# Performance work log

Measured on AMD Instinct MI355X. Metric: run time of the kernel, lower is better.

The kernel has to match this reference:

```python
import jax, jax.numpy as jnp
import numpy as np

# opt constants baked from init_kwargs
OPT_M = 1024      # number of OFDM subcarriers (opt.M)
N_PILOT = 0       # opt.N_pilot
VELOCITY = 100.0  # opt.V (is_random_v=False)
DECAY = 4.0       # opt.decay
C_LIGHT = 3.0e8
CARRIER_FREQ = 3.0e9


def setup_inputs() -> dict:
    key = jax.random.key(0)
    k1, k2 = jax.random.split(key, 2)
    N, P, L, M, S = 16, 4, 16, OPT_M, 128
    # channel tap power profile: exp(-l/decay), normalized
    power = jnp.exp(-jnp.arange(L, dtype=jnp.float32) / DECAY)
    power = power / jnp.sum(power)
    # Rayleigh(sigma=1) samples = sqrt(g1^2 + g2^2), g_i ~ N(0,1)
    g = jax.random.normal(k1, (N, P, L, 2), dtype=jnp.float32)
    rayleigh = jnp.sqrt(g[..., 0] ** 2 + g[..., 1] ** 2)
    cof = jnp.sqrt(power / 2.0) * rayleigh  # (N,P,L), strictly positive
    input_ri = jax.random.normal(k2, (N, P, S * M, 2), dtype=jnp.float32)
    return {"input_ri": input_ri, "cof": cof, "Ns": 128}


def reference(input_ri, cof, Ns):
    N, P, SMK, _ = input_ri.shape
    L = cof.shape[-1]
    S = Ns + N_PILOT  # OFDM mode: S = Ns + N_pilot, M = opt.M
    Mk = SMK // S
    x = (input_ri[..., 0] + 1j * input_ri[..., 1]).astype(jnp.complex64)  # (N,P,SMK)

    # per-tap propagation delay from tap gain: len = -100*log(cof); delay1 = len/c
    delay1 = (-100.0 * jnp.log(cof)) / C_LIGHT                      # (N,P,L)
    delay2 = jnp.linspace(0.0, (S - 1) * (0.0005 / 14.0), S).astype(jnp.float32)  # (S,)
    delay = delay1[..., None] + delay2                              # (N,P,L,S)

    max_doppler = VELOCITY / C_LIGHT * CARRIER_FREQ
    angles = jnp.linspace(0.0, 2.0 * np.pi, L).astype(jnp.float32)  # (L,)
    phase_coef = (2.0 * np.pi * jnp.cos(angles) * max_doppler)      # (L,)
    phases = phase_coef[None, None, :, None] * delay                # (N,P,L,S)
    shift = jnp.exp(-1j * phases.astype(jnp.float32))               # complex64 (N,P,L,S)

    # sum over taps L BEFORE multiplying by the L-independent input (same math,
    # avoids materializing the (N,P,L,S,M) broadcast intermediate)
    factor = jnp.sum(cof[..., None].astype(jnp.complex64) * shift, axis=2)  # (N,P,S)
    out = x.reshape(N, P, S, Mk) * factor[..., None]                # (N,P,S,M)
    out = out.reshape(N, P, SMK)
    out_ri = jnp.stack([out.real, out.imag], axis=-1)               # (N,P,SMK,2)

    # frequency response H_t = FFT of zero-padded taps
    cof_zp = jnp.concatenate([cof, jnp.zeros((N, P, OPT_M - L), cof.dtype)], axis=-1)
    H_t = jnp.fft.fft(cof_zp.astype(jnp.complex64), axis=-1)        # (N,P,OPT_M)
    H_t_ri = jnp.stack([H_t.real, H_t.imag], axis=-1)
    return out_ri, H_t_ri
```

## Files before the change

kernel.cpp:

```cpp
#include <hip/hip_runtime.h>
#include <math.h>

#define NB     16
#define PB     4
#define LTAPS  16
#define SS     128
#define MM     1024

#define TWO_PI_F 6.28318530717958647692f

#define STREAM_BLKS 2048
#define HT_BLKS     256
#define TOT4 (NB * PB * SS * MM / 2)

__global__ __launch_bounds__(256) void fused_kernel(
    const float* __restrict__ in,
    const float* __restrict__ cof,
    float* __restrict__ out,
    float* __restrict__ ht)
{
    const int b = blockIdx.x;
    const int t = threadIdx.x;

    if (b < STREAM_BLKS) {
        __shared__ float term_re[128], term_im[128];
        __shared__ float2 facs[8];

        const int base = b >> 1;
        if (t < 128) {
            const int k  = t >> 4;
            const int l  = t & 15;
            const int id = base + k * 1024;
            const int np = id >> 7;
            const int s  = id & (SS - 1);
            const float cofl   = cof[np * LTAPS + l];
            const float delay1 = (-100.0f / 3.0e8f) * logf(cofl);
            const float delay2 = (0.0005f / 14.0f) * (float)s;
            const float pc     = TWO_PI_F * 1000.0f * cosf((TWO_PI_F / 15.0f) * (float)l);
            const float ph     = pc * (delay1 + delay2);
            float sn, cs;
            sincosf(ph, &sn, &cs);
            term_re[t] = cofl * cs;
            term_im[t] = -cofl * sn;
        }
        __syncthreads();
        if (t < 8) {
            float re = 0.0f, im = 0.0f;
#pragma unroll
            for (int l = 0; l < LTAPS; ++l) {
                re += term_re[t * 16 + l];
                im += term_im[t * 16 + l];
            }
            facs[t] = make_float2(re, im);
        }
        __syncthreads();

        const float4* __restrict__ in4  = (const float4*)in;
        float4* __restrict__       out4 = (float4*)out;
        int g = b * 256 + t;
#pragma unroll
        for (int k = 0; k < 8; ++k, g += STREAM_BLKS * 256) {
            const float2 f = facs[k];
            const float4 v = in4[g];
            float4 r;
            r.x = v.x * f.x - v.y * f.y;
            r.y = v.x * f.y + v.y * f.x;
            r.z = v.z * f.x - v.w * f.y;
            r.w = v.z * f.y + v.w * f.x;
            out4[g] = r;
        }
    } else {
        const int id = (b - STREAM_BLKS) * 256 + t;
        const int np = id >> 10;
        const int k  = id & (MM - 1);
        float sn, cs;
        sincosf((TWO_PI_F / (float)MM) * (float)k, &sn, &cs);
        const float wr = cs, wi = -sn;
        const float* __restrict__ c = cof + np * LTAPS;
        float hr = 0.0f, hi = 0.0f;
        float cr = 1.0f, ci = 0.0f;
#pragma unroll
        for (int l = 0; l < LTAPS; ++l) {
            const float cl = c[l];
            hr += cl * cr;
            hi += cl * ci;
            const float nr = cr * wr - ci * wi;
            const float ni = cr * wi + ci * wr;
            cr = nr; ci = ni;
        }
        ((float2*)ht)[id] = make_float2(hr, hi);
    }
}

extern "C" void kernel_launch(void* const* d_in, const int* in_sizes, int n_in,
                              void* d_out, int out_size, void* d_ws, size_t ws_size,
                              hipStream_t stream)
{
    const float* in  = (const float*)d_in[0];
    const float* cof = (const float*)d_in[1];
    float* out = (float*)d_out;
    float* ht  = out + (size_t)NB * PB * SS * MM * 2;

    hipLaunchKernelGGL(fused_kernel, dim3(STREAM_BLKS + HT_BLKS), dim3(256), 0, stream,
                       in, cof, out, ht);
}
```

Before: 28.66 us.

## Contiguous per-block streaming with nontemporal loads/stores and HT blocks first

Each streaming block now processes a contiguous 32KB chunk covering four (n,p,s) rows, computing four phase factors instead of eight strided ones. Loads and stores use nontemporal builtins to avoid cache pollution on the pure streaming traffic. The small FFT blocks are moved to the front of the grid so they are scheduled early instead of trailing. The contiguous mapping changes DRAM access locality per block compared with the previous grid-strided layout.

```diff
diff --git a/kernel.cpp b/kernel.cpp
--- a/kernel.cpp
+++ b/kernel.cpp
@@ -9,9 +9,12 @@
 
 #define TWO_PI_F 6.28318530717958647692f
 
+#define HT_BLKS     256
 #define STREAM_BLKS 2048
-#define HT_BLKS     256
 #define TOT4 (NB * PB * SS * MM / 2)
+
+typedef float f32x4 __attribute__((ext_vector_type(4)));
+typedef float f32x2 __attribute__((ext_vector_type(2)));
 
 __global__ __launch_bounds__(256) void fused_kernel(
     const float* __restrict__ in,
@@ -22,15 +25,15 @@
     const int b = blockIdx.x;
     const int t = threadIdx.x;
 
-    if (b < STREAM_BLKS) {
-        __shared__ float term_re[128], term_im[128];
-        __shared__ float2 facs[8];
+    if (b >= HT_BLKS) {
+        const int sb = b - HT_BLKS;
+        __shared__ float term_re[64], term_im[64];
+        __shared__ f32x2 facs[4];
 
-        const int base = b >> 1;
-        if (t < 128) {
-            const int k  = t >> 4;
+        if (t < 64) {
+            const int j  = t >> 4;
             const int l  = t & 15;
-            const int id = base + k * 1024;
+            const int id = sb * 4 + j;
             const int np = id >> 7;
             const int s  = id & (SS - 1);
             const float cofl   = cof[np * LTAPS + l];
@@ -44,33 +47,34 @@
             term_im[t] = -cofl * sn;
         }
         __syncthreads();
-        if (t < 8) {
+        if (t < 4) {
             float re = 0.0f, im = 0.0f;
 #pragma unroll
             for (int l = 0; l < LTAPS; ++l) {
                 re += term_re[t * 16 + l];
                 im += term_im[t * 16 + l];
             }
-            facs[t] = make_float2(re, im);
+            f32x2 f; f.x = re; f.y = im;
+            facs[t] = f;
         }
         __syncthreads();
 
-        const float4* __restrict__ in4  = (const float4*)in;
-        float4* __restrict__       out4 = (float4*)out;
-        int g = b * 256 + t;
+        const f32x4* __restrict__ in4  = (const f32x4*)in + (size_t)sb * 2048;
+        f32x4* __restrict__       out4 = (f32x4*)out      + (size_t)sb * 2048;
 #pragma unroll
-        for (int k = 0; k < 8; ++k, g += STREAM_BLKS * 256) {
-            const float2 f = facs[k];
-            const float4 v = in4[g];
-            float4 r;
+        for (int k = 0; k < 8; ++k) {
+            const int   idx = k * 256 + t;
+            const f32x2 f   = facs[k >> 1];
+            const f32x4 v   = __builtin_nontemporal_load(&in4[idx]);
+            f32x4 r;
             r.x = v.x * f.x - v.y * f.y;
             r.y = v.x * f.y + v.y * f.x;
             r.z = v.z * f.x - v.w * f.y;
             r.w = v.z * f.y + v.w * f.x;
-            out4[g] = r;
+            __builtin_nontemporal_store(r, &out4[idx]);
         }
     } else {
-        const int id = (b - STREAM_BLKS) * 256 + t;
+        const int id = b * 256 + t;
         const int np = id >> 10;
         const int k  = id & (MM - 1);
         float sn, cs;
@@ -88,7 +92,8 @@
             const float ni = cr * wi + ci * wr;
             cr = nr; ci = ni;
         }
-        ((float2*)ht)[id] = make_float2(hr, hi);
+        float2* __restrict__ o = (float2*)ht;
+        o[id] = make_float2(hr, hi);
     }
 }
 
@@ -101,6 +106,6 @@
     float* out = (float*)d_out;
     float* ht  = out + (size_t)NB * PB * SS * MM * 2;
 
-    hipLaunchKernelGGL(fused_kernel, dim3(STREAM_BLKS + HT_BLKS), dim3(256), 0, stream,
+    hipLaunchKernelGGL(fused_kernel, dim3(HT_BLKS + STREAM_BLKS), dim3(256), 0, stream,
                        in, cof, out, ht);
 }
```

Result: faster. 26.59 us (-7.2%).
